# Kernel optimization log

Hardware: AMD Instinct MI355X
Metric: run time of the kernel (lower is better)

Reference implementation:

```python
import jax, jax.numpy as jnp
import numpy as np

NUM_HEADS = 16
D_MODEL = 1024
HEAD_DIM = D_MODEL // NUM_HEADS
B, S = 2, 2048


def setup_inputs() -> dict:
    key = jax.random.key(0)
    ks = jax.random.split(key, 11)
    scale = 1.0 / np.sqrt(D_MODEL)
    inp = {
        'query': jax.random.normal(ks[0], (B, S, D_MODEL), jnp.float32),
        'key': jax.random.normal(ks[1], (B, S, D_MODEL), jnp.float32),
        'value': jax.random.normal(ks[2], (B, S, D_MODEL), jnp.float32),
        'Wq': jax.random.normal(ks[3], (D_MODEL, D_MODEL), jnp.float32) * scale,
        'bq': jnp.zeros((D_MODEL,), jnp.float32),
        'Wk': jax.random.normal(ks[4], (D_MODEL, D_MODEL), jnp.float32) * scale,
        'bk': jnp.zeros((D_MODEL,), jnp.float32),
        'Wv': jax.random.normal(ks[5], (D_MODEL, D_MODEL), jnp.float32) * scale,
        'bv': jnp.zeros((D_MODEL,), jnp.float32),
        'Wo': jax.random.normal(ks[6], (D_MODEL, D_MODEL), jnp.float32) * scale,
        'bo': jnp.zeros((D_MODEL,), jnp.float32),
    }
    return inp


def reference(query, key, value, Wq, bq, Wk, bk, Wv, bv, Wo, bo):
    b, s, _ = query.shape
    # Linear projections (torch Linear: x @ W.T + b; here W stored as [in,out])
    Q = query @ Wq + bq
    K = key @ Wk + bk
    V = value @ Wv + bv
    # [B, H, S, Dh]
    Q = Q.reshape(b, s, NUM_HEADS, HEAD_DIM).transpose(0, 2, 1, 3)
    K = K.reshape(b, -1, NUM_HEADS, HEAD_DIM).transpose(0, 2, 1, 3)
    V = V.reshape(b, -1, NUM_HEADS, HEAD_DIM).transpose(0, 2, 1, 3)
    scores = jnp.einsum('bhqd,bhkd->bhqk', Q, K) / jnp.sqrt(jnp.float32(HEAD_DIM)).astype(Q.dtype)
    attn = jax.nn.softmax(scores, axis=-1)
    ctx = jnp.einsum('bhqk,bhkd->bhqd', attn, V)
    ctx = ctx.transpose(0, 2, 1, 3).reshape(b, s, D_MODEL)
    return ctx @ Wo + bo
```

## Files before the change

### kernel.cpp

```cpp
#include <hip/hip_runtime.h>
#include <hip/hip_bf16.h>
#include <math.h>

#define NUM_HEADS 16
#define D_MODEL 1024
#define HEAD_DIM 64
#define BATCH 2
#define SEQ 2048
#define M_TOTAL (BATCH*SEQ)

typedef __bf16 bf16;
typedef __bf16 bf16x2 __attribute__((ext_vector_type(2)));
typedef __bf16 bf16x4 __attribute__((ext_vector_type(4)));
typedef __bf16 bf16x8 __attribute__((ext_vector_type(8)));
typedef float  floatx4 __attribute__((ext_vector_type(4)));

#define CLSCALE 0.180336884f

__device__ __forceinline__ void async_copy16(const bf16* g, bf16* l) {
    __builtin_amdgcn_global_load_lds(
        (const __attribute__((address_space(1))) void*)g,
        (__attribute__((address_space(3))) void*)l, 16, 0, 0);
}

__global__ __launch_bounds__(256)
void convert_w_kernel(const float* __restrict__ Wq, const float* __restrict__ Wk,
                      const float* __restrict__ Wv, const float* __restrict__ Wo,
                      bf16* __restrict__ Wt)
{
    const int z = blockIdx.z;
    const float* W = (z == 0) ? Wq : (z == 1) ? Wk : (z == 2) ? Wv : Wo;
    bf16* dstM = Wt + (size_t)z * D_MODEL * D_MODEL;

    const int n  = blockIdx.x * 256 + threadIdx.x;
    const int k0 = blockIdx.y * 64;
    bf16* dst = dstM + (size_t)n * D_MODEL + k0;

    #pragma unroll
    for (int jc = 0; jc < 8; ++jc) {
        bf16x8 w;
        #pragma unroll
        for (int j = 0; j < 8; ++j)
            w[j] = (bf16)W[(size_t)(k0 + jc * 8 + j) * D_MODEL + n];
        *(bf16x8*)(dst + jc * 8) = w;
    }
}

__global__ __launch_bounds__(256)
void convert_x_kernel(const float* __restrict__ q, const float* __restrict__ k,
                      const float* __restrict__ v, bf16* __restrict__ Xb)
{
    const int z = blockIdx.z;
    const float* X = (z == 0) ? q : (z == 1) ? k : v;
    bf16* dst = Xb + (size_t)z * M_TOTAL * D_MODEL;
    size_t i = ((size_t)blockIdx.x * 256 + threadIdx.x) * 8;
    const float4 u = *(const float4*)(X + i);
    const float4 w = *(const float4*)(X + i + 4);
    bf16x8 o;
    o[0] = (bf16)u.x; o[1] = (bf16)u.y; o[2] = (bf16)u.z; o[3] = (bf16)u.w;
    o[4] = (bf16)w.x; o[5] = (bf16)w.y; o[6] = (bf16)w.z; o[7] = (bf16)w.w;
    *(bf16x8*)(dst + i) = o;
}

__global__ __launch_bounds__(256)
void proj_kernel(const bf16* __restrict__ Xb, const bf16* __restrict__ Wt,
                 const float* __restrict__ bq, const float* __restrict__ bk,
                 const float* __restrict__ bv,
                 bf16* __restrict__ Qo, bf16* __restrict__ Ko, bf16* __restrict__ Vto)
{
    const int which = blockIdx.z;
    const bf16* X     = Xb + (size_t)which * M_TOTAL * D_MODEL;
    const bf16* Wm    = Wt + (size_t)which * D_MODEL * D_MODEL;
    const float* bias = (which == 0) ? bq : (which == 1) ? bk : bv;

    const int tileM = blockIdx.y * 128;
    const int tileN = blockIdx.x * 128;
    const int tid  = threadIdx.x;
    const int lane = tid & 63;
    const int wave = tid >> 6;
    const int quad = lane >> 4;
    const int l16  = lane & 15;

    __shared__ bf16 sA[128 * 32];
    __shared__ bf16 sB[128 * 32];

    floatx4 acc[4][4];
    const floatx4 z4 = {0.0f, 0.0f, 0.0f, 0.0f};
    #pragma unroll
    for (int i = 0; i < 4; i++)
        #pragma unroll
        for (int j = 0; j < 4; j++) acc[i][j] = z4;

    const int wm = (wave >> 1) * 64;
    const int wn = (wave & 1) * 64;

    const int c0   = wave * 64 + lane;
    const int row0 = c0 >> 2, col0 = (c0 & 3) * 8;
    const int c1   = c0 + 256;
    const int row1 = c1 >> 2, col1 = (c1 & 3) * 8;
    bf16* ldsA0 = sA + (size_t)(wave * 64) * 8;
    bf16* ldsA1 = sA + (size_t)(256 + wave * 64) * 8;
    bf16* ldsB0 = sB + (size_t)(wave * 64) * 8;
    bf16* ldsB1 = sB + (size_t)(256 + wave * 64) * 8;

    for (int k0 = 0; k0 < D_MODEL; k0 += 32) {
        __syncthreads();
        async_copy16(X  + (size_t)(tileM + row0) * D_MODEL + k0 + col0, ldsA0);
        async_copy16(X  + (size_t)(tileM + row1) * D_MODEL + k0 + col1, ldsA1);
        async_copy16(Wm + (size_t)(tileN + row0) * D_MODEL + k0 + col0, ldsB0);
        async_copy16(Wm + (size_t)(tileN + row1) * D_MODEL + k0 + col1, ldsB1);
        __syncthreads();

        bf16x8 af[4], bfr[4];
        #pragma unroll
        for (int i = 0; i < 4; i++) af[i]  = *(const bf16x8*)&sA[(wm + i * 16 + l16) * 32 + quad * 8];
        #pragma unroll
        for (int j = 0; j < 4; j++) bfr[j] = *(const bf16x8*)&sB[(wn + j * 16 + l16) * 32 + quad * 8];
        if (which != 2) {
            #pragma unroll
            for (int i = 0; i < 4; i++)
                #pragma unroll
                for (int j = 0; j < 4; j++)
                    acc[i][j] = __builtin_amdgcn_mfma_f32_16x16x32_bf16(af[i], bfr[j], acc[i][j], 0, 0, 0);
        } else {
            #pragma unroll
            for (int i = 0; i < 4; i++)
                #pragma unroll
                for (int j = 0; j < 4; j++)
                    acc[i][j] = __builtin_amdgcn_mfma_f32_16x16x32_bf16(bfr[i], af[j], acc[i][j], 0, 0, 0);
        }
    }

    if (which != 2) {
        bf16* out = (which == 0) ? Qo : Ko;
        const float oscale = (which == 0) ? CLSCALE : 1.0f;
        #pragma unroll
        for (int i = 0; i < 4; i++) {
            int mbase = tileM + wm + i * 16 + quad * 4;
            #pragma unroll
            for (int j = 0; j < 4; j++) {
                int n = tileN + wn + j * 16 + l16;
                float bb = bias[n];
                int h = n >> 6, d = n & 63;
                #pragma unroll
                for (int r = 0; r < 4; r++) {
                    int mm = mbase + r;
                    int b = mm >> 11, s = mm & 2047;
                    out[(((size_t)(b * NUM_HEADS + h)) * SEQ + s) * HEAD_DIM + d] =
                        (bf16)((acc[i][j][r] + bb) * oscale);
                }
            }
        }
    } else {
        #pragma unroll
        for (int i = 0; i < 4; i++) {
            #pragma unroll
            for (int r = 0; r < 4; r++) {
                int n = tileN + wn + i * 16 + quad * 4 + r;
                float bb = bias[n];
                int h = n >> 6, d = n & 63;
                #pragma unroll
                for (int j = 0; j < 4; j++) {
                    int m = tileM + wm + j * 16 + l16;
                    int b = m >> 11, s = m & 2047;
                    Vto[(((size_t)(b * NUM_HEADS + h)) * HEAD_DIM + d) * SEQ + s] =
                        (bf16)(acc[i][j][r] + bb);
                }
            }
        }
    }
}

__global__ __launch_bounds__(256)
void attn_kernel(const bf16* __restrict__ Q, const bf16* __restrict__ K,
                 const bf16* __restrict__ Vt, bf16* __restrict__ Ctx)
{
    const int bh  = blockIdx.y;
    const int b   = bh >> 4, h = bh & 15;
    const int q0  = blockIdx.x * 64;
    const int tid = threadIdx.x;
    const int lane = tid & 63;
    const int wave = tid >> 6;
    const int quad = lane >> 4;
    const int l16  = lane & 15;

    __shared__ bf16 sQ[64][72];
    __shared__ bf16 sK[64][72];
    __shared__ bf16 sVt[64][72];
    __shared__ bf16 sP[64][72];

    const bf16* Qb  = Q  + ((size_t)bh * SEQ + q0) * HEAD_DIM;
    const bf16* Kb  = K  + (size_t)bh * SEQ * HEAD_DIM;
    const bf16* Vtb = Vt + (size_t)bh * HEAD_DIM * SEQ;

    #pragma unroll
    for (int it = 0; it < 2; ++it) {
        int g   = tid + it * 256;
        int row = g >> 3;
        int c   = (g & 7) * 8;
        *(bf16x8*)&sQ[row][c] = *(const bf16x8*)(Qb + (size_t)row * HEAD_DIM + c);
    }
    __syncthreads();

    const int m0 = wave * 16;
    bf16x8 bQ[2];
    bQ[0] = *(const bf16x8*)&sQ[m0 + l16][quad * 8];
    bQ[1] = *(const bf16x8*)&sQ[m0 + l16][32 + quad * 8];

    floatx4 o[4];
    const floatx4 z4 = {0.0f, 0.0f, 0.0f, 0.0f};
    #pragma unroll
    for (int t = 0; t < 4; t++) o[t] = z4;
    floatx4 lpart = z4;

    for (int kt = 0; kt < SEQ / 64; ++kt) {
        __syncthreads();
        #pragma unroll
        for (int it = 0; it < 2; ++it) {
            int g   = tid + it * 256;
            int row = g >> 3;
            int c   = (g & 7) * 8;
            *(bf16x8*)&sK[row][c] =
                *(const bf16x8*)(Kb + ((size_t)(kt * 64 + row)) * HEAD_DIM + c);
        }
        #pragma unroll
        for (int it = 0; it < 2; ++it) {
            int g = tid + it * 256;
            int d = g >> 3;
            int c = (g & 7) * 8;
            *(bf16x8*)&sVt[d][c] =
                *(const bf16x8*)(Vtb + (size_t)d * SEQ + kt * 64 + c);
        }
        __syncthreads();

        floatx4 sc[4];
        #pragma unroll
        for (int t = 0; t < 4; t++) {
            bf16x8 a0 = *(const bf16x8*)&sK[t * 16 + l16][quad * 8];
            bf16x8 a1 = *(const bf16x8*)&sK[t * 16 + l16][32 + quad * 8];
            floatx4 z = z4;
            z = __builtin_amdgcn_mfma_f32_16x16x32_bf16(a0, bQ[0], z, 0, 0, 0);
            z = __builtin_amdgcn_mfma_f32_16x16x32_bf16(a1, bQ[1], z, 0, 0, 0);
            sc[t] = z;
        }

        #pragma unroll
        for (int t = 0; t < 4; t++)
            #pragma unroll
            for (int r = 0; r < 4; r++)
                sc[t][r] = exp2f(sc[t][r]);
        lpart += sc[0] + sc[1] + sc[2] + sc[3];

        #pragma unroll
        for (int t = 0; t < 4; t++) {
            bf16x4 pk;
            #pragma unroll
            for (int r = 0; r < 4; r++) pk[r] = (bf16)sc[t][r];
            *(bf16x4*)&sP[m0 + l16][t * 16 + quad * 4] = pk;
        }

        bf16x8 bP0 = *(const bf16x8*)&sP[m0 + l16][quad * 8];
        bf16x8 bP1 = *(const bf16x8*)&sP[m0 + l16][32 + quad * 8];
        #pragma unroll
        for (int dt = 0; dt < 4; dt++) {
            bf16x8 a0 = *(const bf16x8*)&sVt[dt * 16 + l16][quad * 8];
            bf16x8 a1 = *(const bf16x8*)&sVt[dt * 16 + l16][32 + quad * 8];
            o[dt] = __builtin_amdgcn_mfma_f32_16x16x32_bf16(a0, bP0, o[dt], 0, 0, 0);
            o[dt] = __builtin_amdgcn_mfma_f32_16x16x32_bf16(a1, bP1, o[dt], 0, 0, 0);
        }
    }

    float rs = (lpart[0] + lpart[1]) + (lpart[2] + lpart[3]);
    rs += __shfl_xor(rs, 16, 64);
    rs += __shfl_xor(rs, 32, 64);
    float inv = 1.0f / rs;

    int q = q0 + m0 + l16;
    size_t base = ((size_t)b * SEQ + q) * D_MODEL + h * HEAD_DIM;
    #pragma unroll
    for (int dt = 0; dt < 4; dt++) {
        bf16x4 w;
        #pragma unroll
        for (int r = 0; r < 4; r++) w[r] = (bf16)(o[dt][r] * inv);
        *(bf16x4*)&Ctx[base + dt * 16 + quad * 4] = w;
    }
}

__global__ __launch_bounds__(256)
void out_proj_kernel(const bf16* __restrict__ A, const bf16* __restrict__ Wto,
                     const float* __restrict__ bias, float* __restrict__ Out)
{
    const int tileM = blockIdx.y * 64;
    const int tileN = blockIdx.x * 128;
    const int tid  = threadIdx.x;
    const int lane = tid & 63;
    const int wave = tid >> 6;
    const int quad = lane >> 4;
    const int l16  = lane & 15;

    __shared__ bf16 sA[64 * 32];
    __shared__ bf16 sB[128 * 32];

    floatx4 acc[2][4];
    const floatx4 z4 = {0.0f, 0.0f, 0.0f, 0.0f};
    #pragma unroll
    for (int i = 0; i < 2; i++)
        #pragma unroll
        for (int j = 0; j < 4; j++) acc[i][j] = z4;

    const int wm = (wave >> 1) * 32;
    const int wn = (wave & 1) * 64;

    const int c0   = wave * 64 + lane;
    const int row0 = c0 >> 2, col0 = (c0 & 3) * 8;
    const int c1   = c0 + 256;
    const int row1 = c1 >> 2, col1 = (c1 & 3) * 8;
    bf16* ldsA0 = sA + (size_t)(wave * 64) * 8;
    bf16* ldsB0 = sB + (size_t)(wave * 64) * 8;
    bf16* ldsB1 = sB + (size_t)(256 + wave * 64) * 8;

    for (int k0 = 0; k0 < D_MODEL; k0 += 32) {
        __syncthreads();
        async_copy16(A   + (size_t)(tileM + row0) * D_MODEL + k0 + col0, ldsA0);
        async_copy16(Wto + (size_t)(tileN + row0) * D_MODEL + k0 + col0, ldsB0);
        async_copy16(Wto + (size_t)(tileN + row1) * D_MODEL + k0 + col1, ldsB1);
        __syncthreads();

        bf16x8 af[2], bfr[4];
        #pragma unroll
        for (int i = 0; i < 2; i++) af[i]  = *(const bf16x8*)&sA[(wm + i * 16 + l16) * 32 + quad * 8];
        #pragma unroll
        for (int j = 0; j < 4; j++) bfr[j] = *(const bf16x8*)&sB[(wn + j * 16 + l16) * 32 + quad * 8];
        #pragma unroll
        for (int i = 0; i < 2; i++)
            #pragma unroll
            for (int j = 0; j < 4; j++)
                acc[i][j] = __builtin_amdgcn_mfma_f32_16x16x32_bf16(af[i], bfr[j], acc[i][j], 0, 0, 0);
    }

    #pragma unroll
    for (int i = 0; i < 2; i++) {
        int mbase = tileM + wm + i * 16 + quad * 4;
        #pragma unroll
        for (int j = 0; j < 4; j++) {
            int n = tileN + wn + j * 16 + l16;
            float bb = bias[n];
            #pragma unroll
            for (int r = 0; r < 4; r++)
                Out[(size_t)(mbase + r) * D_MODEL + n] = acc[i][j][r] + bb;
        }
    }
}

extern "C" void kernel_launch(void* const* d_in, const int* in_sizes, int n_in,
                              void* d_out, int out_size, void* d_ws, size_t ws_size,
                              hipStream_t stream)
{
    const float* q  = (const float*)d_in[0];
    const float* k  = (const float*)d_in[1];
    const float* v  = (const float*)d_in[2];
    const float* Wq = (const float*)d_in[3];
    const float* bq = (const float*)d_in[4];
    const float* Wk = (const float*)d_in[5];
    const float* bk = (const float*)d_in[6];
    const float* Wv = (const float*)d_in[7];
    const float* bv = (const float*)d_in[8];
    const float* Wo = (const float*)d_in[9];
    const float* bo = (const float*)d_in[10];
    float* out = (float*)d_out;

    const size_t PLANE = (size_t)M_TOTAL * D_MODEL;
    bf16* Qb = (bf16*)d_ws;
    bf16* Kb = Qb + PLANE;
    bf16* Vt = Kb + PLANE;
    bf16* Cb = Vt + PLANE;
    bf16* Wt = Cb + PLANE;
    bf16* Xb = Wt + 4 * (size_t)D_MODEL * D_MODEL;

    convert_w_kernel<<<dim3(4, 16, 4), 256, 0, stream>>>(Wq, Wk, Wv, Wo, Wt);
    convert_x_kernel<<<dim3(2048, 1, 3), 256, 0, stream>>>(q, k, v, Xb);
    proj_kernel<<<dim3(8, 32, 3), 256, 0, stream>>>(Xb, Wt, bq, bk, bv, Qb, Kb, Vt);
    attn_kernel<<<dim3(32, 32), 256, 0, stream>>>(Qb, Kb, Vt, Cb);
    out_proj_kernel<<<dim3(8, 64), 256, 0, stream>>>(Cb, Wt + 3 * (size_t)D_MODEL * D_MODEL, bo, out);
}
```

Baseline: 260.1 us.

## Process 128 queries per attention block with two query tiles per wave

Each wave now handles two 16-row query tiles, so each K and V tile loaded into shared memory is reused across 128 queries instead of 64. This halves the global and LDS traffic for K/V per query. The P staging buffer aliases the Q shared array to keep LDS usage down. The cost is a halved grid and more accumulator registers per thread, which can lower occupancy.

```diff
diff --git a/kernel.cpp b/kernel.cpp
--- a/kernel.cpp
+++ b/kernel.cpp
@@ -177,41 +177,45 @@
 {
     const int bh  = blockIdx.y;
     const int b   = bh >> 4, h = bh & 15;
-    const int q0  = blockIdx.x * 64;
+    const int q0  = blockIdx.x * 128;
     const int tid = threadIdx.x;
     const int lane = tid & 63;
     const int wave = tid >> 6;
     const int quad = lane >> 4;
     const int l16  = lane & 15;
 
-    __shared__ bf16 sQ[64][72];
+    __shared__ bf16 sQP[128][72];
     __shared__ bf16 sK[64][72];
     __shared__ bf16 sVt[64][72];
-    __shared__ bf16 sP[64][72];
 
     const bf16* Qb  = Q  + ((size_t)bh * SEQ + q0) * HEAD_DIM;
     const bf16* Kb  = K  + (size_t)bh * SEQ * HEAD_DIM;
     const bf16* Vtb = Vt + (size_t)bh * HEAD_DIM * SEQ;
 
     #pragma unroll
-    for (int it = 0; it < 2; ++it) {
+    for (int it = 0; it < 4; ++it) {
         int g   = tid + it * 256;
         int row = g >> 3;
         int c   = (g & 7) * 8;
-        *(bf16x8*)&sQ[row][c] = *(const bf16x8*)(Qb + (size_t)row * HEAD_DIM + c);
+        *(bf16x8*)&sQP[row][c] = *(const bf16x8*)(Qb + (size_t)row * HEAD_DIM + c);
     }
     __syncthreads();
 
-    const int m0 = wave * 16;
-    bf16x8 bQ[2];
-    bQ[0] = *(const bf16x8*)&sQ[m0 + l16][quad * 8];
-    bQ[1] = *(const bf16x8*)&sQ[m0 + l16][32 + quad * 8];
-
-    floatx4 o[4];
+    const int wq = wave * 32;
+    bf16x8 bQ[2][2];
+    #pragma unroll
+    for (int qt = 0; qt < 2; qt++) {
+        bQ[qt][0] = *(const bf16x8*)&sQP[wq + qt * 16 + l16][quad * 8];
+        bQ[qt][1] = *(const bf16x8*)&sQP[wq + qt * 16 + l16][32 + quad * 8];
+    }
+
+    floatx4 o[2][4];
     const floatx4 z4 = {0.0f, 0.0f, 0.0f, 0.0f};
     #pragma unroll
-    for (int t = 0; t < 4; t++) o[t] = z4;
-    floatx4 lpart = z4;
+    for (int qt = 0; qt < 2; qt++)
+        #pragma unroll
+        for (int t = 0; t < 4; t++) o[qt][t] = z4;
+    floatx4 lpart[2] = {z4, z4};
 
     for (int kt = 0; kt < SEQ / 64; ++kt) {
         __syncthreads();
@@ -233,56 +237,75 @@
         }
         __syncthreads();
 
-        floatx4 sc[4];
+        floatx4 sc[2][4];
         #pragma unroll
         for (int t = 0; t < 4; t++) {
             bf16x8 a0 = *(const bf16x8*)&sK[t * 16 + l16][quad * 8];
             bf16x8 a1 = *(const bf16x8*)&sK[t * 16 + l16][32 + quad * 8];
-            floatx4 z = z4;
-            z = __builtin_amdgcn_mfma_f32_16x16x32_bf16(a0, bQ[0], z, 0, 0, 0);
-            z = __builtin_amdgcn_mfma_f32_16x16x32_bf16(a1, bQ[1], z, 0, 0, 0);
-            sc[t] = z;
-        }
-
-        #pragma unroll
-        for (int t = 0; t < 4; t++)
-            #pragma unroll
-            for (int r = 0; r < 4; r++)
-                sc[t][r] = exp2f(sc[t][r]);
-        lpart += sc[0] + sc[1] + sc[2] + sc[3];
-
-        #pragma unroll
-        for (int t = 0; t < 4; t++) {
-            bf16x4 pk;
-            #pragma unroll
-            for (int r = 0; r < 4; r++) pk[r] = (bf16)sc[t][r];
-            *(bf16x4*)&sP[m0 + l16][t * 16 + quad * 4] = pk;
-        }
-
-        bf16x8 bP0 = *(const bf16x8*)&sP[m0 + l16][quad * 8];
-        bf16x8 bP1 = *(const bf16x8*)&sP[m0 + l16][32 + quad * 8];
+            #pragma unroll
+            for (int qt = 0; qt < 2; qt++) {
+                floatx4 z = z4;
+                z = __builtin_amdgcn_mfma_f32_16x16x32_bf16(a0, bQ[qt][0], z, 0, 0, 0);
+                z = __builtin_amdgcn_mfma_f32_16x16x32_bf16(a1, bQ[qt][1], z, 0, 0, 0);
+                sc[qt][t] = z;
+            }
+        }
+
+        #pragma unroll
+        for (int qt = 0; qt < 2; qt++) {
+            #pragma unroll
+            for (int t = 0; t < 4; t++)
+                #pragma unroll
+                for (int r = 0; r < 4; r++)
+                    sc[qt][t][r] = exp2f(sc[qt][t][r]);
+            lpart[qt] += sc[qt][0] + sc[qt][1] + sc[qt][2] + sc[qt][3];
+        }
+
+        #pragma unroll
+        for (int qt = 0; qt < 2; qt++)
+            #pragma unroll
+            for (int t = 0; t < 4; t++) {
+                bf16x4 pk;
+                #pragma unroll
+                for (int r = 0; r < 4; r++) pk[r] = (bf16)sc[qt][t][r];
+                *(bf16x4*)&sQP[wq + qt * 16 + l16][t * 16 + quad * 4] = pk;
+            }
+
+        bf16x8 bP[2][2];
+        #pragma unroll
+        for (int qt = 0; qt < 2; qt++) {
+            bP[qt][0] = *(const bf16x8*)&sQP[wq + qt * 16 + l16][quad * 8];
+            bP[qt][1] = *(const bf16x8*)&sQP[wq + qt * 16 + l16][32 + quad * 8];
+        }
+
         #pragma unroll
         for (int dt = 0; dt < 4; dt++) {
             bf16x8 a0 = *(const bf16x8*)&sVt[dt * 16 + l16][quad * 8];
             bf16x8 a1 = *(const bf16x8*)&sVt[dt * 16 + l16][32 + quad * 8];
-            o[dt] = __builtin_amdgcn_mfma_f32_16x16x32_bf16(a0, bP0, o[dt], 0, 0, 0);
-            o[dt] = __builtin_amdgcn_mfma_f32_16x16x32_bf16(a1, bP1, o[dt], 0, 0, 0);
-        }
-    }
-
-    float rs = (lpart[0] + lpart[1]) + (lpart[2] + lpart[3]);
-    rs += __shfl_xor(rs, 16, 64);
-    rs += __shfl_xor(rs, 32, 64);
-    float inv = 1.0f / rs;
-
-    int q = q0 + m0 + l16;
-    size_t base = ((size_t)b * SEQ + q) * D_MODEL + h * HEAD_DIM;
-    #pragma unroll
-    for (int dt = 0; dt < 4; dt++) {
-        bf16x4 w;
-        #pragma unroll
-        for (int r = 0; r < 4; r++) w[r] = (bf16)(o[dt][r] * inv);
-        *(bf16x4*)&Ctx[base + dt * 16 + quad * 4] = w;
+            #pragma unroll
+            for (int qt = 0; qt < 2; qt++) {
+                o[qt][dt] = __builtin_amdgcn_mfma_f32_16x16x32_bf16(a0, bP[qt][0], o[qt][dt], 0, 0, 0);
+                o[qt][dt] = __builtin_amdgcn_mfma_f32_16x16x32_bf16(a1, bP[qt][1], o[qt][dt], 0, 0, 0);
+            }
+        }
+    }
+
+    #pragma unroll
+    for (int qt = 0; qt < 2; qt++) {
+        float rs = (lpart[qt][0] + lpart[qt][1]) + (lpart[qt][2] + lpart[qt][3]);
+        rs += __shfl_xor(rs, 16, 64);
+        rs += __shfl_xor(rs, 32, 64);
+        float inv = 1.0f / rs;
+
+        int q = q0 + wq + qt * 16 + l16;
+        size_t base = ((size_t)b * SEQ + q) * D_MODEL + h * HEAD_DIM;
+        #pragma unroll
+        for (int dt = 0; dt < 4; dt++) {
+            bf16x4 w;
+            #pragma unroll
+            for (int r = 0; r < 4; r++) w[r] = (bf16)(o[qt][dt][r] * inv);
+            *(bf16x4*)&Ctx[base + dt * 16 + quad * 4] = w;
+        }
     }
 }
 
@@ -380,6 +403,6 @@
     convert_w_kernel<<<dim3(4, 16, 4), 256, 0, stream>>>(Wq, Wk, Wv, Wo, Wt);
     convert_x_kernel<<<dim3(2048, 1, 3), 256, 0, stream>>>(q, k, v, Xb);
     proj_kernel<<<dim3(8, 32, 3), 256, 0, stream>>>(Xb, Wt, bq, bk, bv, Qb, Kb, Vt);
-    attn_kernel<<<dim3(32, 32), 256, 0, stream>>>(Qb, Kb, Vt, Cb);
+    attn_kernel<<<dim3(16, 32), 256, 0, stream>>>(Qb, Kb, Vt, Cb);
     out_proj_kernel<<<dim3(8, 64), 256, 0, stream>>>(Cb, Wt + 3 * (size_t)D_MODEL * D_MODEL, bo, out);
 }
```

Measured after the change: 272.9 us. +4.9%, slower.

## Merge convert kernels, XCD-aware attention grid, async swizzled K/V LDS loads

Applied to the files above, without the earlier changes.

Fuses the weight and activation conversion kernels into a single launch. Remaps the attention grid so that blocks sharing a batch-head land on the same XCD, aiming for better L2 reuse of K/V. K and V tiles are now loaded with global_load_lds async copies into unpadded, XOR-swizzled LDS to avoid register round trips and bank conflicts, and the Q buffer is reused for P to save LDS. Each iteration still syncs with no double buffering, so load latency is not hidden.

```diff
diff --git a/kernel.cpp b/kernel.cpp
--- a/kernel.cpp
+++ b/kernel.cpp
@@ -24,42 +24,46 @@
 }
 
 __global__ __launch_bounds__(256)
-void convert_w_kernel(const float* __restrict__ Wq, const float* __restrict__ Wk,
-                      const float* __restrict__ Wv, const float* __restrict__ Wo,
-                      bf16* __restrict__ Wt)
-{
-    const int z = blockIdx.z;
-    const float* W = (z == 0) ? Wq : (z == 1) ? Wk : (z == 2) ? Wv : Wo;
-    bf16* dstM = Wt + (size_t)z * D_MODEL * D_MODEL;
-
-    const int n  = blockIdx.x * 256 + threadIdx.x;
-    const int k0 = blockIdx.y * 64;
-    bf16* dst = dstM + (size_t)n * D_MODEL + k0;
-
-    #pragma unroll
-    for (int jc = 0; jc < 8; ++jc) {
-        bf16x8 w;
-        #pragma unroll
-        for (int j = 0; j < 8; ++j)
-            w[j] = (bf16)W[(size_t)(k0 + jc * 8 + j) * D_MODEL + n];
-        *(bf16x8*)(dst + jc * 8) = w;
-    }
-}
-
-__global__ __launch_bounds__(256)
-void convert_x_kernel(const float* __restrict__ q, const float* __restrict__ k,
-                      const float* __restrict__ v, bf16* __restrict__ Xb)
-{
-    const int z = blockIdx.z;
-    const float* X = (z == 0) ? q : (z == 1) ? k : v;
-    bf16* dst = Xb + (size_t)z * M_TOTAL * D_MODEL;
-    size_t i = ((size_t)blockIdx.x * 256 + threadIdx.x) * 8;
-    const float4 u = *(const float4*)(X + i);
-    const float4 w = *(const float4*)(X + i + 4);
-    bf16x8 o;
-    o[0] = (bf16)u.x; o[1] = (bf16)u.y; o[2] = (bf16)u.z; o[3] = (bf16)u.w;
-    o[4] = (bf16)w.x; o[5] = (bf16)w.y; o[6] = (bf16)w.z; o[7] = (bf16)w.w;
-    *(bf16x8*)(dst + i) = o;
+void convert_kernel(const float* __restrict__ Wq, const float* __restrict__ Wk,
+                    const float* __restrict__ Wv, const float* __restrict__ Wo,
+                    const float* __restrict__ q, const float* __restrict__ k,
+                    const float* __restrict__ v,
+                    bf16* __restrict__ Wt, bf16* __restrict__ Xb)
+{
+    const int blk = blockIdx.x;
+    const int tid = threadIdx.x;
+    if (blk < 256) {
+        const int wi  = blk >> 6;
+        const int sub = blk & 63;
+        const int xb  = sub & 3;
+        const int yb  = sub >> 2;
+        const float* W = (wi == 0) ? Wq : (wi == 1) ? Wk : (wi == 2) ? Wv : Wo;
+        bf16* dstM = Wt + (size_t)wi * D_MODEL * D_MODEL;
+        const int n  = xb * 256 + tid;
+        const int k0 = yb * 64;
+        bf16* dst = dstM + (size_t)n * D_MODEL + k0;
+        #pragma unroll
+        for (int jc = 0; jc < 8; ++jc) {
+            bf16x8 w;
+            #pragma unroll
+            for (int j = 0; j < 8; ++j)
+                w[j] = (bf16)W[(size_t)(k0 + jc * 8 + j) * D_MODEL + n];
+            *(bf16x8*)(dst + jc * 8) = w;
+        }
+    } else {
+        const int rem   = blk - 256;
+        const int plane = rem >> 11;
+        const int xb    = rem & 2047;
+        const float* X = (plane == 0) ? q : (plane == 1) ? k : v;
+        bf16* dst = Xb + (size_t)plane * M_TOTAL * D_MODEL;
+        size_t i = ((size_t)xb * 256 + tid) * 8;
+        const float4 u = *(const float4*)(X + i);
+        const float4 w = *(const float4*)(X + i + 4);
+        bf16x8 o;
+        o[0] = (bf16)u.x; o[1] = (bf16)u.y; o[2] = (bf16)u.z; o[3] = (bf16)u.w;
+        o[4] = (bf16)w.x; o[5] = (bf16)w.y; o[6] = (bf16)w.z; o[7] = (bf16)w.w;
+        *(bf16x8*)(dst + i) = o;
+    }
 }
 
 __global__ __launch_bounds__(256)
@@ -175,19 +179,24 @@
 void attn_kernel(const bf16* __restrict__ Q, const bf16* __restrict__ K,
                  const bf16* __restrict__ Vt, bf16* __restrict__ Ctx)
 {
-    const int bh  = blockIdx.y;
-    const int b   = bh >> 4, h = bh & 15;
-    const int q0  = blockIdx.x * 64;
+    const int lin    = blockIdx.x;
+    const int xcd    = lin & 7;
+    const int rest   = lin >> 3;
+    const int superg = rest >> 5;
+    const int qi     = rest & 31;
+    const int bh     = superg * 8 + xcd;
+    const int b      = bh >> 4, h = bh & 15;
+    const int q0     = qi * 64;
+
     const int tid = threadIdx.x;
     const int lane = tid & 63;
     const int wave = tid >> 6;
     const int quad = lane >> 4;
     const int l16  = lane & 15;
 
-    __shared__ bf16 sQ[64][72];
-    __shared__ bf16 sK[64][72];
-    __shared__ bf16 sVt[64][72];
-    __shared__ bf16 sP[64][72];
+    __shared__ bf16 sQP[64][72];
+    __shared__ bf16 sK[64 * 64];
+    __shared__ bf16 sVt[64 * 64];
 
     const bf16* Qb  = Q  + ((size_t)bh * SEQ + q0) * HEAD_DIM;
     const bf16* Kb  = K  + (size_t)bh * SEQ * HEAD_DIM;
@@ -198,14 +207,14 @@
         int g   = tid + it * 256;
         int row = g >> 3;
         int c   = (g & 7) * 8;
-        *(bf16x8*)&sQ[row][c] = *(const bf16x8*)(Qb + (size_t)row * HEAD_DIM + c);
+        *(bf16x8*)&sQP[row][c] = *(const bf16x8*)(Qb + (size_t)row * HEAD_DIM + c);
     }
     __syncthreads();
 
     const int m0 = wave * 16;
     bf16x8 bQ[2];
-    bQ[0] = *(const bf16x8*)&sQ[m0 + l16][quad * 8];
-    bQ[1] = *(const bf16x8*)&sQ[m0 + l16][32 + quad * 8];
+    bQ[0] = *(const bf16x8*)&sQP[m0 + l16][quad * 8];
+    bQ[1] = *(const bf16x8*)&sQP[m0 + l16][32 + quad * 8];
 
     floatx4 o[4];
     const floatx4 z4 = {0.0f, 0.0f, 0.0f, 0.0f};
@@ -213,31 +222,30 @@
     for (int t = 0; t < 4; t++) o[t] = z4;
     floatx4 lpart = z4;
 
+    const int xs = l16 & 7;
+    const int cho0 = ((quad)     ^ xs) * 8;
+    const int cho1 = ((4 + quad) ^ xs) * 8;
+
     for (int kt = 0; kt < SEQ / 64; ++kt) {
         __syncthreads();
         #pragma unroll
         for (int it = 0; it < 2; ++it) {
-            int g   = tid + it * 256;
-            int row = g >> 3;
-            int c   = (g & 7) * 8;
-            *(bf16x8*)&sK[row][c] =
-                *(const bf16x8*)(Kb + ((size_t)(kt * 64 + row)) * HEAD_DIM + c);
-        }
-        #pragma unroll
-        for (int it = 0; it < 2; ++it) {
-            int g = tid + it * 256;
-            int d = g >> 3;
-            int c = (g & 7) * 8;
-            *(bf16x8*)&sVt[d][c] =
-                *(const bf16x8*)(Vtb + (size_t)d * SEQ + kt * 64 + c);
+            int c    = tid + it * 256;
+            int row  = c >> 3;
+            int scol = ((c & 7) ^ (row & 7)) * 8;
+            async_copy16(Kb  + (size_t)(kt * 64 + row) * HEAD_DIM + scol,
+                         sK + (size_t)c * 8);
+            async_copy16(Vtb + (size_t)row * SEQ + kt * 64 + scol,
+                         sVt + (size_t)c * 8);
         }
         __syncthreads();
 
         floatx4 sc[4];
         #pragma unroll
         for (int t = 0; t < 4; t++) {
-            bf16x8 a0 = *(const bf16x8*)&sK[t * 16 + l16][quad * 8];
-            bf16x8 a1 = *(const bf16x8*)&sK[t * 16 + l16][32 + quad * 8];
+            const int ra = (t * 16 + l16) * 64;
+            bf16x8 a0 = *(const bf16x8*)&sK[ra + cho0];
+            bf16x8 a1 = *(const bf16x8*)&sK[ra + cho1];
             floatx4 z = z4;
             z = __builtin_amdgcn_mfma_f32_16x16x32_bf16(a0, bQ[0], z, 0, 0, 0);
             z = __builtin_amdgcn_mfma_f32_16x16x32_bf16(a1, bQ[1], z, 0, 0, 0);
@@ -256,15 +264,17 @@
             bf16x4 pk;
             #pragma unroll
             for (int r = 0; r < 4; r++) pk[r] = (bf16)sc[t][r];
-            *(bf16x4*)&sP[m0 + l16][t * 16 + quad * 4] = pk;
-        }
-
-        bf16x8 bP0 = *(const bf16x8*)&sP[m0 + l16][quad * 8];
-        bf16x8 bP1 = *(const bf16x8*)&sP[m0 + l16][32 + quad * 8];
+            *(bf16x4*)&sQP[m0 + l16][t * 16 + quad * 4] = pk;
+        }
+
+        bf16x8 bP0 = *(const bf16x8*)&sQP[m0 + l16][quad * 8];
+        bf16x8 bP1 = *(const bf16x8*)&sQP[m0 + l16][32 + quad * 8];
+
         #pragma unroll
         for (int dt = 0; dt < 4; dt++) {
-            bf16x8 a0 = *(const bf16x8*)&sVt[dt * 16 + l16][quad * 8];
-            bf16x8 a1 = *(const bf16x8*)&sVt[dt * 16 + l16][32 + quad * 8];
+            const int ra = (dt * 16 + l16) * 64;
+            bf16x8 a0 = *(const bf16x8*)&sVt[ra + cho0];
+            bf16x8 a1 = *(const bf16x8*)&sVt[ra + cho1];
             o[dt] = __builtin_amdgcn_mfma_f32_16x16x32_bf16(a0, bP0, o[dt], 0, 0, 0);
             o[dt] = __builtin_amdgcn_mfma_f32_16x16x32_bf16(a1, bP1, o[dt], 0, 0, 0);
         }
@@ -275,8 +285,8 @@
     rs += __shfl_xor(rs, 32, 64);
     float inv = 1.0f / rs;
 
-    int q = q0 + m0 + l16;
-    size_t base = ((size_t)b * SEQ + q) * D_MODEL + h * HEAD_DIM;
+    int qq = q0 + m0 + l16;
+    size_t base = ((size_t)b * SEQ + qq) * D_MODEL + h * HEAD_DIM;
     #pragma unroll
     for (int dt = 0; dt < 4; dt++) {
         bf16x4 w;
@@ -377,9 +387,8 @@
     bf16* Wt = Cb + PLANE;
     bf16* Xb = Wt + 4 * (size_t)D_MODEL * D_MODEL;
 
-    convert_w_kernel<<<dim3(4, 16, 4), 256, 0, stream>>>(Wq, Wk, Wv, Wo, Wt);
-    convert_x_kernel<<<dim3(2048, 1, 3), 256, 0, stream>>>(q, k, v, Xb);
+    convert_kernel<<<dim3(6400), 256, 0, stream>>>(Wq, Wk, Wv, Wo, q, k, v, Wt, Xb);
     proj_kernel<<<dim3(8, 32, 3), 256, 0, stream>>>(Xb, Wt, bq, bk, bv, Qb, Kb, Vt);
-    attn_kernel<<<dim3(32, 32), 256, 0, stream>>>(Qb, Kb, Vt, Cb);
+    attn_kernel<<<dim3(1024), 256, 0, stream>>>(Qb, Kb, Vt, Cb);
     out_proj_kernel<<<dim3(8, 64), 256, 0, stream>>>(Cb, Wt + 3 * (size_t)D_MODEL * D_MODEL, bo, out);
 }
```

After: 258.2 us. No clear change (-0.7%).
